# Kernel optimization log

Hardware: AMD Instinct MI355X
Metric: run time of the kernel (lower is better)

Reference implementation:

```python
import jax, jax.numpy as jnp
import numpy as np

V, E, U, D = 32000, 128, 256, 256
B, T = 128, 1024


def setup_inputs() -> dict:
    key = jax.random.key(0)
    k_tok, k_emb, k_wk, k_wr, k_wd = jax.random.split(key, 5)
    tokens = jax.random.randint(k_tok, (B, T), 0, V, dtype=jnp.int32)
    emb_table = jax.random.normal(k_emb, (V, E), dtype=jnp.float32) * 0.02
    Wk = jax.random.normal(k_wk, (E, 4 * U), dtype=jnp.float32) * (1.0 / np.sqrt(E))
    Wr = jax.random.normal(k_wr, (U, 4 * U), dtype=jnp.float32) * (1.0 / np.sqrt(U))
    # Keras unit_forget_bias: forget-gate bias initialized to ones (gate order i,f,g,o)
    b = jnp.concatenate([jnp.zeros((U,), jnp.float32), jnp.ones((U,), jnp.float32), jnp.zeros((2 * U,), jnp.float32)])
    Wd = jax.random.normal(k_wd, (U, D), dtype=jnp.float32) * (1.0 / np.sqrt(U))
    bd = jnp.zeros((D,), jnp.float32)
    return {"tokens": tokens, "emb_table": emb_table, "Wk": Wk, "Wr": Wr, "b": b, "Wd": Wd, "bd": bd}


def _masked_lstm(x, mask, Wk, Wr, b):
    # x: [B,T,E], mask: [B,T] bool. Keras semantics: masked steps pass
    # previous h as output and leave (h, c) unchanged.
    units = Wr.shape[0]
    bsz = x.shape[0]
    xT = jnp.swapaxes(x, 0, 1)          # [T,B,E]
    mT = jnp.swapaxes(mask, 0, 1)       # [T,B]

    def step(carry, inp):
        h, c = carry
        xt, mt = inp
        z = xt @ Wk + h @ Wr + b        # [B,4U]
        i, f, g, o = jnp.split(z, 4, axis=-1)
        i = jax.nn.sigmoid(i)
        f = jax.nn.sigmoid(f)
        g = jnp.tanh(g)
        o = jax.nn.sigmoid(o)
        c_new = f * c + i * g
        h_new = o * jnp.tanh(c_new)
        m = mt[:, None]
        h2 = jnp.where(m, h_new, h)
        c2 = jnp.where(m, c_new, c)
        return (h2, c2), h2

    h0 = jnp.zeros((bsz, units), x.dtype)
    c0 = jnp.zeros((bsz, units), x.dtype)
    _, outs = jax.lax.scan(step, (h0, c0), (xT, mT))
    return jnp.swapaxes(outs, 0, 1)     # [B,T,U]


def reference(tokens, emb_table, Wk, Wr, b, Wd, bd):
    # Embedding (mask_zero=True); dropout layers are identity at inference.
    x = emb_table[tokens]               # [B,T,E]
    mask = tokens != 0                  # [B,T]
    h = _masked_lstm(x, mask, Wk, Wr, b)  # [B,T,U]
    y = jax.nn.relu(h @ Wd + bd)        # TimeDistributed Dense(relu) -> [B,T,D]
    return y
```

## Files before the change

kernel.cpp:

```cpp
#include <hip/hip_runtime.h>
#include <cstddef>


typedef unsigned int u32x4 __attribute__((ext_vector_type(4)));

constexpr int TLEN = 1024;
constexpr int EDIM = 128;
constexpr int UDIM = 256;
constexpr int DDIM = 256;

constexpr int NBG  = 16;
constexpr int BPB  = 8;
constexpr int UPB  = 8;
constexpr int ZCOL = 32;
constexpr int HXROW = 432;
constexpr int ZROW = 36;

__device__ unsigned long long g_pktA[2][128][256];
__device__ unsigned long long g_pktB[2][128][256];
__device__ unsigned           g_cnt[NBG][32];

__device__ __forceinline__ int pidx(int k) { return ((k >> 5) * 36) + (k & 31); }

__device__ __forceinline__ u32x4 pkt_load_ic(const unsigned long long* p) {
  u32x4 v;
  asm volatile("global_load_dwordx4 %0, %1, off sc0 sc1" : "=v"(v) : "v"(p));
  return v;
}
__device__ __forceinline__ u32x4 pkt_load_l2(const unsigned long long* p) {
  u32x4 v;
  asm volatile("global_load_dwordx4 %0, %1, off sc0" : "=v"(v) : "v"(p));
  return v;
}
__device__ __forceinline__ unsigned cnt_load_ic(const unsigned* p) {
  unsigned v;
  asm volatile("global_load_dword %0, %1, off sc0 sc1" : "=v"(v) : "v"(p));
  asm volatile("s_waitcnt vmcnt(0)" : "+v"(v) :: "memory");
  return v;
}
#define PKT_WAIT4(a, b, c, d) \
  asm volatile("s_waitcnt vmcnt(0)" : "+v"(a), "+v"(b), "+v"(c), "+v"(d) :: "memory")
#define TAGS_OK() \
  ((p0[1] == want) & (p0[3] == want) & (p1[1] == want) & (p1[3] == want) & \
   (p2[1] == want) & (p2[3] == want) & (p3[1] == want) & (p3[3] == want))

__device__ __forceinline__ float rowsum16(float v) {
  v += __int_as_float(
      __builtin_amdgcn_mov_dpp(__float_as_int(v), 0x121, 0xf, 0xf, true));
  v += __int_as_float(
      __builtin_amdgcn_mov_dpp(__float_as_int(v), 0x122, 0xf, 0xf, true));
  v += __int_as_float(
      __builtin_amdgcn_mov_dpp(__float_as_int(v), 0x124, 0xf, 0xf, true));
  v += __int_as_float(
      __builtin_amdgcn_mov_dpp(__float_as_int(v), 0x128, 0xf, 0xf, true));
  return v;
}

__global__ void we_init() {
  const int i = blockIdx.x * 256 + threadIdx.x;
  if (i < NBG * 32)
    __hip_atomic_store(&(&g_cnt[0][0])[i], 0u, __ATOMIC_RELAXED,
                       __HIP_MEMORY_SCOPE_AGENT);
}

__global__ __launch_bounds__(256, 2) void we_lstm(
    const int* __restrict__ tokens, const float* __restrict__ emb,
    const float* __restrict__ Wk, const float* __restrict__ Wr,
    const float* __restrict__ bz, float* __restrict__ out)
{
  __shared__ float hx[2][BPB][HXROW];
  __shared__ float zs[BPB][ZROW];
  __shared__ float bias_s[ZCOL];

  const int tid = threadIdx.x;
  const int bid = blockIdx.x;
  const int bg  = ((bid & 7) << 1) | ((bid >> 8) & 1);
  const int ug  = (bid >> 3) & 31;
  const int b0  = bg * BPB;
  const int u0  = ug * UPB;

  const int ksl = tid & 15;
  const int cq  = (tid >> 4) & 7;
  const int bh  = tid >> 7;

  float w[96];
#pragma unroll
  for (int i = 0; i < 6; ++i)
#pragma unroll
    for (int j = 0; j < 4; ++j) {
      const int k = ksl * 4 + i * 64 + j;
#pragma unroll
      for (int cc = 0; cc < 4; ++cc) {
        const int c   = cq * 4 + cc;
        const int col = ((c >> 3) << 8) + u0 + (c & 7);
        w[(i * 4 + j) * 4 + cc] =
            (k < UDIM) ? Wr[k * 1024 + col] : Wk[(k - UDIM) * 1024 + col];
      }
    }
  if (tid < ZCOL) bias_s[tid] = bz[((tid >> 3) << 8) + u0 + (tid & 7)];

  float creg = 0.f;
  const int gb = tid >> 3, gu = tid & 7;
  const int xb = tid >> 5, xe = (tid & 31) << 2;
  const int up = tid & 127, bq = (tid >> 7) * 4;

  bool use_local = true;

  float4 xv = *(const float4*)&emb[(size_t)tokens[(b0 + xb) * TLEN] * EDIM + xe];
  int tk_g = (tid < 64) ? tokens[(b0 + gb) * TLEN] : 1;

  for (int it = 0; it < TLEN; ++it) {
    const int cur = it & 1;

    *(float4*)&hx[cur][xb][pidx(UDIM + xe)] = xv;
    __syncthreads();

    float acc[4][4];
#pragma unroll
    for (int r = 0; r < 4; ++r) {
      acc[r][0] = 0.f; acc[r][1] = 0.f; acc[r][2] = 0.f; acc[r][3] = 0.f;
    }
#pragma unroll
    for (int i = 4; i < 6; ++i) {
      const int hoff = pidx(ksl * 4 + i * 64);
      float4 hv[4];
#pragma unroll
      for (int r = 0; r < 4; ++r)
        hv[r] = *(const float4*)&hx[cur][bh * 4 + r][hoff];
#pragma unroll
      for (int j = 0; j < 4; ++j)
#pragma unroll
        for (int r = 0; r < 4; ++r) {
          const float hval = (j == 0) ? hv[r].x : (j == 1) ? hv[r].y
                             : (j == 2) ? hv[r].z : hv[r].w;
#pragma unroll
          for (int cc = 0; cc < 4; ++cc)
            acc[r][cc] += hval * w[(i * 4 + j) * 4 + cc];
        }
    }

    u32x4 p0, p1, p2, p3;
    const unsigned want = (unsigned)it;
    const int rp = (it + 1) & 1;
    if (it > 0) {
      if (use_local) {
        p0 = pkt_load_l2(&g_pktA[rp][b0 + bq + 0][2 * up]);
        p1 = pkt_load_l2(&g_pktA[rp][b0 + bq + 1][2 * up]);
        p2 = pkt_load_l2(&g_pktA[rp][b0 + bq + 2][2 * up]);
        p3 = pkt_load_l2(&g_pktA[rp][b0 + bq + 3][2 * up]);
      } else {
        p0 = pkt_load_ic(&g_pktB[rp][b0 + bq + 0][2 * up]);
        p1 = pkt_load_ic(&g_pktB[rp][b0 + bq + 1][2 * up]);
        p2 = pkt_load_ic(&g_pktB[rp][b0 + bq + 2][2 * up]);
        p3 = pkt_load_ic(&g_pktB[rp][b0 + bq + 3][2 * up]);
      }
    }

    float4 xv_n;
    int tk_g_n = 1;
    if (it + 1 < TLEN) {
      const int tk_x = tokens[(b0 + xb) * TLEN + it + 1];
      xv_n = *(const float4*)&emb[(size_t)tk_x * EDIM + xe];
      if (tid < 64) tk_g_n = tokens[(b0 + gb) * TLEN + it + 1];
    }

    const int ho = pidx(2 * up);
    if (it > 0) {
      PKT_WAIT4(p0, p1, p2, p3);
      bool ok = TAGS_OK();
      if (!ok) {
        const unsigned wantc = 32u * (unsigned)it;
        while (cnt_load_ic(&g_cnt[bg][0]) < wantc)
          __builtin_amdgcn_s_sleep(1);
        if (use_local) {
          p0 = pkt_load_l2(&g_pktA[rp][b0 + bq + 0][2 * up]);
          p1 = pkt_load_l2(&g_pktA[rp][b0 + bq + 1][2 * up]);
          p2 = pkt_load_l2(&g_pktA[rp][b0 + bq + 2][2 * up]);
          p3 = pkt_load_l2(&g_pktA[rp][b0 + bq + 3][2 * up]);
          PKT_WAIT4(p0, p1, p2, p3);
          ok = TAGS_OK();
          if (!ok) use_local = false;
        }
        while (!ok) {
          p0 = pkt_load_ic(&g_pktB[rp][b0 + bq + 0][2 * up]);
          p1 = pkt_load_ic(&g_pktB[rp][b0 + bq + 1][2 * up]);
          p2 = pkt_load_ic(&g_pktB[rp][b0 + bq + 2][2 * up]);
          p3 = pkt_load_ic(&g_pktB[rp][b0 + bq + 3][2 * up]);
          PKT_WAIT4(p0, p1, p2, p3);
          ok = TAGS_OK();
          if (!ok) __builtin_amdgcn_s_sleep(1);
        }
      }
      *(float2*)&hx[cur][bq + 0][ho] =
          make_float2(__uint_as_float(p0[0]), __uint_as_float(p0[2]));
      *(float2*)&hx[cur][bq + 1][ho] =
          make_float2(__uint_as_float(p1[0]), __uint_as_float(p1[2]));
      *(float2*)&hx[cur][bq + 2][ho] =
          make_float2(__uint_as_float(p2[0]), __uint_as_float(p2[2]));
      *(float2*)&hx[cur][bq + 3][ho] =
          make_float2(__uint_as_float(p3[0]), __uint_as_float(p3[2]));
    } else {
#pragma unroll
      for (int jj = 0; jj < 4; ++jj)
        *(float2*)&hx[cur][bq + jj][ho] = make_float2(0.f, 0.f);
    }
    __syncthreads();

#pragma unroll
    for (int i = 0; i < 4; ++i) {
      const int hoff = pidx(ksl * 4 + i * 64);
      float4 hv[4];
#pragma unroll
      for (int r = 0; r < 4; ++r)
        hv[r] = *(const float4*)&hx[cur][bh * 4 + r][hoff];
#pragma unroll
      for (int j = 0; j < 4; ++j)
#pragma unroll
        for (int r = 0; r < 4; ++r) {
          const float hval = (j == 0) ? hv[r].x : (j == 1) ? hv[r].y
                             : (j == 2) ? hv[r].z : hv[r].w;
#pragma unroll
          for (int cc = 0; cc < 4; ++cc)
            acc[r][cc] += hval * w[(i * 4 + j) * 4 + cc];
        }
    }

#pragma unroll
    for (int r = 0; r < 4; ++r)
#pragma unroll
      for (int cc = 0; cc < 4; ++cc)
        acc[r][cc] = rowsum16(acc[r][cc]);
    if (ksl == 0) {
#pragma unroll
      for (int r = 0; r < 4; ++r)
        *(float4*)&zs[bh * 4 + r][cq * 4] =
            make_float4(acc[r][0], acc[r][1], acc[r][2], acc[r][3]);
    }
    __syncthreads();

    if (tid < 64) {
      const float zi = zs[gb][gu]      + bias_s[gu];
      const float zf = zs[gb][8 + gu]  + bias_s[8 + gu];
      const float zg = zs[gb][16 + gu] + bias_s[16 + gu];
      const float zo = zs[gb][24 + gu] + bias_s[24 + gu];
      const float gi = 1.f / (1.f + __expf(-zi));
      const float gf = 1.f / (1.f + __expf(-zf));
      const float gg = 1.f - 2.f / (1.f + __expf(2.f * zg));
      const float go = 1.f / (1.f + __expf(-zo));
      const float cn = gf * creg + gi * gg;
      const float th = 1.f - 2.f / (1.f + __expf(2.f * cn));
      const float hn = go * th;
      const bool msk = (tk_g != 0);
      const float hold = hx[cur][gb][pidx(u0 + gu)];
      const float h2 = msk ? hn : hold;
      creg = msk ? cn : creg;
      const unsigned long long pkt =
          ((unsigned long long)(unsigned)(it + 1) << 32) | __float_as_uint(h2);
      __hip_atomic_store(&g_pktA[cur][b0 + gb][u0 + gu], pkt, __ATOMIC_RELAXED,
                         __HIP_MEMORY_SCOPE_WORKGROUP);
      __hip_atomic_store(&g_pktB[cur][b0 + gb][u0 + gu], pkt, __ATOMIC_RELAXED,
                         __HIP_MEMORY_SCOPE_AGENT);
      __builtin_nontemporal_store(
          h2, &out[((size_t)(b0 + gb) * TLEN + it) * DDIM + u0 + gu]);
      asm volatile("s_waitcnt vmcnt(0)" ::: "memory");
      if (tid == 0)
        __hip_atomic_fetch_add(&g_cnt[bg][0], 1u, __ATOMIC_RELAXED,
                               __HIP_MEMORY_SCOPE_AGENT);
    }
    xv = xv_n;
    tk_g = tk_g_n;
  }
}

__global__ __launch_bounds__(256, 2) void we_proj(
    const float* __restrict__ Wd, const float* __restrict__ bd,
    float* __restrict__ out)
{
  __shared__ float hs[32][260];
  __shared__ float ws[32][260];
  __shared__ float bds[DDIM];

  const int tid = threadIdx.x;
  const size_t row0 = (size_t)blockIdx.x * 32;

#pragma unroll
  for (int j2 = 0; j2 < 8; ++j2) {
    const int idx = tid + j2 * 256;
    const int r = idx >> 6;
    const int cq = idx & 63;
    *(float4*)&hs[r][cq * 4] = *(const float4*)&out[(row0 + r) * DDIM + cq * 4];
  }
  bds[tid] = bd[tid];

  const int rg = tid >> 5;
  const int c0 = (tid & 31) * 8;
  float acc[4][8];
#pragma unroll
  for (int i = 0; i < 4; ++i)
#pragma unroll
    for (int c = 0; c < 8; ++c) acc[i][c] = 0.f;

  for (int kt = 0; kt < 8; ++kt) {
    __syncthreads();
#pragma unroll
    for (int j2 = 0; j2 < 8; ++j2) {
      const int idx = tid + j2 * 256;
      const int kk = idx >> 6;
      const int cq = idx & 63;
      *(float4*)&ws[kk][cq * 4] =
          *(const float4*)&Wd[(size_t)(kt * 32 + kk) * DDIM + cq * 4];
    }
    __syncthreads();
#pragma unroll
    for (int kk = 0; kk < 32; ++kk) {
      const float4 wv0 = *(const float4*)&ws[kk][c0];
      const float4 wv1 = *(const float4*)&ws[kk][c0 + 4];
#pragma unroll
      for (int i = 0; i < 4; ++i) {
        const float hval = hs[rg + i * 8][kt * 32 + kk];
        acc[i][0] += hval * wv0.x; acc[i][1] += hval * wv0.y;
        acc[i][2] += hval * wv0.z; acc[i][3] += hval * wv0.w;
        acc[i][4] += hval * wv1.x; acc[i][5] += hval * wv1.y;
        acc[i][6] += hval * wv1.z; acc[i][7] += hval * wv1.w;
      }
    }
  }
#pragma unroll
  for (int i = 0; i < 4; ++i) {
    float4 y0, y1;
    y0.x = fmaxf(acc[i][0] + bds[c0 + 0], 0.f);
    y0.y = fmaxf(acc[i][1] + bds[c0 + 1], 0.f);
    y0.z = fmaxf(acc[i][2] + bds[c0 + 2], 0.f);
    y0.w = fmaxf(acc[i][3] + bds[c0 + 3], 0.f);
    y1.x = fmaxf(acc[i][4] + bds[c0 + 4], 0.f);
    y1.y = fmaxf(acc[i][5] + bds[c0 + 5], 0.f);
    y1.z = fmaxf(acc[i][6] + bds[c0 + 6], 0.f);
    y1.w = fmaxf(acc[i][7] + bds[c0 + 7], 0.f);
    const size_t orow = (row0 + rg + i * 8) * DDIM;
    *(float4*)&out[orow + c0]     = y0;
    *(float4*)&out[orow + c0 + 4] = y1;
  }
}

extern "C" void kernel_launch(void* const* d_in, const int* in_sizes, int n_in,
                              void* d_out, int out_size, void* d_ws, size_t ws_size,
                              hipStream_t stream) {
  const int*   tokens = (const int*)d_in[0];
  const float* emb    = (const float*)d_in[1];
  const float* Wk     = (const float*)d_in[2];
  const float* Wr     = (const float*)d_in[3];
  const float* bz     = (const float*)d_in[4];
  const float* Wd     = (const float*)d_in[5];
  const float* bd     = (const float*)d_in[6];
  float* out = (float*)d_out;
  (void)in_sizes; (void)n_in; (void)out_size; (void)d_ws; (void)ws_size;
  hipLaunchKernelGGL(we_init, dim3(2), dim3(256), 0, stream);
  hipLaunchKernelGGL(we_lstm, dim3(512), dim3(256), 0, stream,
                     tokens, emb, Wk, Wr, bz, out);
  hipLaunchKernelGGL(we_proj, dim3(128 * TLEN / 32), dim3(256), 0, stream,
                     Wd, bd, out);
}
```

Before: 3.650 ms.

## Compute gates in registers after reduction and split L2/IC ready counters

Reassigns weight columns so that after the DPP row reduction each lane with ksl<4 holds all four gates for one (batch, unit) pair. This removes the zs shared staging buffer and one __syncthreads per step. Readiness signalling is split into a workgroup-scope L2 counter and an agent-scope IC counter, each bumped per wavefront, with a bounded spin on the local counter before falling back to the coherent path. Half the blocks also sleep briefly at start to stagger them. The price is more atomics per step, each wavefront waiting on vmcnt twice, and more intricate fallback logic.

```diff
diff --git a/kernel.cpp b/kernel.cpp
--- a/kernel.cpp
+++ b/kernel.cpp
@@ -12,13 +12,12 @@
 constexpr int NBG  = 16;
 constexpr int BPB  = 8;
 constexpr int UPB  = 8;
-constexpr int ZCOL = 32;
 constexpr int HXROW = 432;
-constexpr int ZROW = 36;
 
 __device__ unsigned long long g_pktA[2][128][256];
 __device__ unsigned long long g_pktB[2][128][256];
-__device__ unsigned           g_cnt[NBG][32];
+__device__ unsigned           g_cntL[NBG][32];
+__device__ unsigned           g_cntIC[NBG][32];
 
 __device__ __forceinline__ int pidx(int k) { return ((k >> 5) * 36) + (k & 31); }
 
@@ -30,6 +29,12 @@
 __device__ __forceinline__ u32x4 pkt_load_l2(const unsigned long long* p) {
   u32x4 v;
   asm volatile("global_load_dwordx4 %0, %1, off sc0" : "=v"(v) : "v"(p));
+  return v;
+}
+__device__ __forceinline__ unsigned cnt_load_l2(const unsigned* p) {
+  unsigned v;
+  asm volatile("global_load_dword %0, %1, off sc0" : "=v"(v) : "v"(p));
+  asm volatile("s_waitcnt vmcnt(0)" : "+v"(v) :: "memory");
   return v;
 }
 __device__ __forceinline__ unsigned cnt_load_ic(const unsigned* p) {
@@ -58,9 +63,12 @@
 
 __global__ void we_init() {
   const int i = blockIdx.x * 256 + threadIdx.x;
-  if (i < NBG * 32)
-    __hip_atomic_store(&(&g_cnt[0][0])[i], 0u, __ATOMIC_RELAXED,
+  if (i < NBG * 32) {
+    __hip_atomic_store(&(&g_cntL[0][0])[i], 0u, __ATOMIC_RELAXED,
                        __HIP_MEMORY_SCOPE_AGENT);
+    __hip_atomic_store(&(&g_cntIC[0][0])[i], 0u, __ATOMIC_RELAXED,
+                       __HIP_MEMORY_SCOPE_AGENT);
+  }
 }
 
 __global__ __launch_bounds__(256, 2) void we_lstm(
@@ -69,8 +77,6 @@
     const float* __restrict__ bz, float* __restrict__ out)
 {
   __shared__ float hx[2][BPB][HXROW];
-  __shared__ float zs[BPB][ZROW];
-  __shared__ float bias_s[ZCOL];
 
   const int tid = threadIdx.x;
   const int bid = blockIdx.x;
@@ -91,23 +97,29 @@
       const int k = ksl * 4 + i * 64 + j;
 #pragma unroll
       for (int cc = 0; cc < 4; ++cc) {
-        const int c   = cq * 4 + cc;
-        const int col = ((c >> 3) << 8) + u0 + (c & 7);
+        const int col = (cc << 8) + u0 + cq;
         w[(i * 4 + j) * 4 + cc] =
             (k < UDIM) ? Wr[k * 1024 + col] : Wk[(k - UDIM) * 1024 + col];
       }
     }
-  if (tid < ZCOL) bias_s[tid] = bz[((tid >> 3) << 8) + u0 + (tid & 7)];
+  float bias_r[4];
+#pragma unroll
+  for (int cc = 0; cc < 4; ++cc) bias_r[cc] = bz[(cc << 8) + u0 + cq];
 
   float creg = 0.f;
-  const int gb = tid >> 3, gu = tid & 7;
+  const int gbat = bh * 4 + (tid & 3);
   const int xb = tid >> 5, xe = (tid & 31) << 2;
   const int up = tid & 127, bq = (tid >> 7) * 4;
 
   bool use_local = true;
 
   float4 xv = *(const float4*)&emb[(size_t)tokens[(b0 + xb) * TLEN] * EDIM + xe];
-  int tk_g = (tid < 64) ? tokens[(b0 + gb) * TLEN] : 1;
+  int tk_m = tokens[(b0 + gbat) * TLEN];
+
+  if ((bid >> 8) & 1) {
+    __builtin_amdgcn_s_sleep(31);
+    __builtin_amdgcn_s_sleep(31);
+  }
 
   for (int it = 0; it < TLEN; ++it) {
     const int cur = it & 1;
@@ -157,11 +169,11 @@
     }
 
     float4 xv_n;
-    int tk_g_n = 1;
+    int tk_m_n = 1;
     if (it + 1 < TLEN) {
       const int tk_x = tokens[(b0 + xb) * TLEN + it + 1];
       xv_n = *(const float4*)&emb[(size_t)tk_x * EDIM + xe];
-      if (tid < 64) tk_g_n = tokens[(b0 + gb) * TLEN + it + 1];
+      tk_m_n = tokens[(b0 + gbat) * TLEN + it + 1];
     }
 
     const int ho = pidx(2 * up);
@@ -169,26 +181,37 @@
       PKT_WAIT4(p0, p1, p2, p3);
       bool ok = TAGS_OK();
       if (!ok) {
-        const unsigned wantc = 32u * (unsigned)it;
-        while (cnt_load_ic(&g_cnt[bg][0]) < wantc)
-          __builtin_amdgcn_s_sleep(1);
+        const unsigned wantc = 128u * (unsigned)it;
         if (use_local) {
-          p0 = pkt_load_l2(&g_pktA[rp][b0 + bq + 0][2 * up]);
-          p1 = pkt_load_l2(&g_pktA[rp][b0 + bq + 1][2 * up]);
-          p2 = pkt_load_l2(&g_pktA[rp][b0 + bq + 2][2 * up]);
-          p3 = pkt_load_l2(&g_pktA[rp][b0 + bq + 3][2 * up]);
-          PKT_WAIT4(p0, p1, p2, p3);
-          ok = TAGS_OK();
+          int rounds = 0;
+          bool cert = false;
+          while (rounds < 64) {
+            if (cnt_load_l2(&g_cntL[bg][0]) >= wantc) { cert = true; break; }
+            __builtin_amdgcn_s_sleep(1);
+            ++rounds;
+          }
+          if (cert) {
+            p0 = pkt_load_l2(&g_pktA[rp][b0 + bq + 0][2 * up]);
+            p1 = pkt_load_l2(&g_pktA[rp][b0 + bq + 1][2 * up]);
+            p2 = pkt_load_l2(&g_pktA[rp][b0 + bq + 2][2 * up]);
+            p3 = pkt_load_l2(&g_pktA[rp][b0 + bq + 3][2 * up]);
+            PKT_WAIT4(p0, p1, p2, p3);
+            ok = TAGS_OK();
+          }
           if (!ok) use_local = false;
         }
-        while (!ok) {
-          p0 = pkt_load_ic(&g_pktB[rp][b0 + bq + 0][2 * up]);
-          p1 = pkt_load_ic(&g_pktB[rp][b0 + bq + 1][2 * up]);
-          p2 = pkt_load_ic(&g_pktB[rp][b0 + bq + 2][2 * up]);
-          p3 = pkt_load_ic(&g_pktB[rp][b0 + bq + 3][2 * up]);
-          PKT_WAIT4(p0, p1, p2, p3);
-          ok = TAGS_OK();
-          if (!ok) __builtin_amdgcn_s_sleep(1);
+        if (!ok) {
+          while (cnt_load_ic(&g_cntIC[bg][0]) < wantc)
+            __builtin_amdgcn_s_sleep(1);
+          do {
+            p0 = pkt_load_ic(&g_pktB[rp][b0 + bq + 0][2 * up]);
+            p1 = pkt_load_ic(&g_pktB[rp][b0 + bq + 1][2 * up]);
+            p2 = pkt_load_ic(&g_pktB[rp][b0 + bq + 2][2 * up]);
+            p3 = pkt_load_ic(&g_pktB[rp][b0 + bq + 3][2 * up]);
+            PKT_WAIT4(p0, p1, p2, p3);
+            ok = TAGS_OK();
+            if (!ok) __builtin_amdgcn_s_sleep(1);
+          } while (!ok);
         }
       }
       *(float2*)&hx[cur][bq + 0][ho] =
@@ -230,45 +253,47 @@
 #pragma unroll
       for (int cc = 0; cc < 4; ++cc)
         acc[r][cc] = rowsum16(acc[r][cc]);
-    if (ksl == 0) {
-#pragma unroll
-      for (int r = 0; r < 4; ++r)
-        *(float4*)&zs[bh * 4 + r][cq * 4] =
-            make_float4(acc[r][0], acc[r][1], acc[r][2], acc[r][3]);
-    }
-    __syncthreads();
-
-    if (tid < 64) {
-      const float zi = zs[gb][gu]      + bias_s[gu];
-      const float zf = zs[gb][8 + gu]  + bias_s[8 + gu];
-      const float zg = zs[gb][16 + gu] + bias_s[16 + gu];
-      const float zo = zs[gb][24 + gu] + bias_s[24 + gu];
-      const float gi = 1.f / (1.f + __expf(-zi));
-      const float gf = 1.f / (1.f + __expf(-zf));
-      const float gg = 1.f - 2.f / (1.f + __expf(2.f * zg));
-      const float go = 1.f / (1.f + __expf(-zo));
+
+    const bool pub = (ksl < 4);
+    unsigned long long pkt = 0;
+    float h2 = 0.f;
+    if (pub) {
+      float z4[4];
+#pragma unroll
+      for (int cc = 0; cc < 4; ++cc)
+        z4[cc] = ((ksl == 0) ? acc[0][cc] : (ksl == 1) ? acc[1][cc]
+                  : (ksl == 2) ? acc[2][cc] : acc[3][cc]) + bias_r[cc];
+      const float gi = 1.f / (1.f + __expf(-z4[0]));
+      const float gf = 1.f / (1.f + __expf(-z4[1]));
+      const float gg = 1.f - 2.f / (1.f + __expf(2.f * z4[2]));
+      const float go = 1.f / (1.f + __expf(-z4[3]));
       const float cn = gf * creg + gi * gg;
       const float th = 1.f - 2.f / (1.f + __expf(2.f * cn));
       const float hn = go * th;
-      const bool msk = (tk_g != 0);
-      const float hold = hx[cur][gb][pidx(u0 + gu)];
-      const float h2 = msk ? hn : hold;
+      const bool msk = (tk_m != 0);
+      const float hold = hx[cur][gbat][pidx(u0 + cq)];
+      h2 = msk ? hn : hold;
       creg = msk ? cn : creg;
-      const unsigned long long pkt =
-          ((unsigned long long)(unsigned)(it + 1) << 32) | __float_as_uint(h2);
-      __hip_atomic_store(&g_pktA[cur][b0 + gb][u0 + gu], pkt, __ATOMIC_RELAXED,
-                         __HIP_MEMORY_SCOPE_WORKGROUP);
-      __hip_atomic_store(&g_pktB[cur][b0 + gb][u0 + gu], pkt, __ATOMIC_RELAXED,
-                         __HIP_MEMORY_SCOPE_AGENT);
+      pkt = ((unsigned long long)(unsigned)(it + 1) << 32) | __float_as_uint(h2);
+      __hip_atomic_store(&g_pktA[cur][b0 + gbat][u0 + cq], pkt,
+                         __ATOMIC_RELAXED, __HIP_MEMORY_SCOPE_WORKGROUP);
+    }
+    asm volatile("s_waitcnt vmcnt(0)" ::: "memory");
+    if ((tid & 63) == 0)
+      __hip_atomic_fetch_add(&g_cntL[bg][0], 1u, __ATOMIC_RELAXED,
+                             __HIP_MEMORY_SCOPE_WORKGROUP);
+    if (pub)
+      __hip_atomic_store(&g_pktB[cur][b0 + gbat][u0 + cq], pkt,
+                         __ATOMIC_RELAXED, __HIP_MEMORY_SCOPE_AGENT);
+    asm volatile("s_waitcnt vmcnt(0)" ::: "memory");
+    if ((tid & 63) == 0)
+      __hip_atomic_fetch_add(&g_cntIC[bg][0], 1u, __ATOMIC_RELAXED,
+                             __HIP_MEMORY_SCOPE_AGENT);
+    if (pub)
       __builtin_nontemporal_store(
-          h2, &out[((size_t)(b0 + gb) * TLEN + it) * DDIM + u0 + gu]);
-      asm volatile("s_waitcnt vmcnt(0)" ::: "memory");
-      if (tid == 0)
-        __hip_atomic_fetch_add(&g_cnt[bg][0], 1u, __ATOMIC_RELAXED,
-                               __HIP_MEMORY_SCOPE_AGENT);
-    }
+          h2, &out[((size_t)(b0 + gbat) * TLEN + it) * DDIM + u0 + cq]);
     xv = xv_n;
-    tk_g = tk_g_n;
+    tk_m = tk_m_n;
   }
 }
 
```

After: 7.585 ms. 108% more time.

## Split step counter into local-L2 and cross-die counters for faster handoff

Applied to the files above, without the earlier changes.

Replaces the single agent-scope arrival counter with two counters. One is bumped right after the workgroup-scope (local L2) packet store and polled with L2-only loads for a bounded number of rounds. The other is the existing agent-scope counter, bumped after the coherent store and used as a fallback. The aim is to let consumers on the same XCD see readiness without waiting on the slower infinity-cache-coherent path. The cost is an extra waitcnt and atomic on the producer side per step, plus a bounded spin that may add latency when the producers are remote.

```diff
diff --git a/kernel.cpp b/kernel.cpp
--- a/kernel.cpp
+++ b/kernel.cpp
@@ -18,7 +18,8 @@
 
 __device__ unsigned long long g_pktA[2][128][256];
 __device__ unsigned long long g_pktB[2][128][256];
-__device__ unsigned           g_cnt[NBG][32];
+__device__ unsigned           g_cntL[NBG][32];
+__device__ unsigned           g_cntIC[NBG][32];
 
 __device__ __forceinline__ int pidx(int k) { return ((k >> 5) * 36) + (k & 31); }
 
@@ -30,6 +31,12 @@
 __device__ __forceinline__ u32x4 pkt_load_l2(const unsigned long long* p) {
   u32x4 v;
   asm volatile("global_load_dwordx4 %0, %1, off sc0" : "=v"(v) : "v"(p));
+  return v;
+}
+__device__ __forceinline__ unsigned cnt_load_l2(const unsigned* p) {
+  unsigned v;
+  asm volatile("global_load_dword %0, %1, off sc0" : "=v"(v) : "v"(p));
+  asm volatile("s_waitcnt vmcnt(0)" : "+v"(v) :: "memory");
   return v;
 }
 __device__ __forceinline__ unsigned cnt_load_ic(const unsigned* p) {
@@ -58,9 +65,12 @@
 
 __global__ void we_init() {
   const int i = blockIdx.x * 256 + threadIdx.x;
-  if (i < NBG * 32)
-    __hip_atomic_store(&(&g_cnt[0][0])[i], 0u, __ATOMIC_RELAXED,
+  if (i < NBG * 32) {
+    __hip_atomic_store(&(&g_cntL[0][0])[i], 0u, __ATOMIC_RELAXED,
                        __HIP_MEMORY_SCOPE_AGENT);
+    __hip_atomic_store(&(&g_cntIC[0][0])[i], 0u, __ATOMIC_RELAXED,
+                       __HIP_MEMORY_SCOPE_AGENT);
+  }
 }
 
 __global__ __launch_bounds__(256, 2) void we_lstm(
@@ -170,25 +180,36 @@
       bool ok = TAGS_OK();
       if (!ok) {
         const unsigned wantc = 32u * (unsigned)it;
-        while (cnt_load_ic(&g_cnt[bg][0]) < wantc)
-          __builtin_amdgcn_s_sleep(1);
         if (use_local) {
-          p0 = pkt_load_l2(&g_pktA[rp][b0 + bq + 0][2 * up]);
-          p1 = pkt_load_l2(&g_pktA[rp][b0 + bq + 1][2 * up]);
-          p2 = pkt_load_l2(&g_pktA[rp][b0 + bq + 2][2 * up]);
-          p3 = pkt_load_l2(&g_pktA[rp][b0 + bq + 3][2 * up]);
-          PKT_WAIT4(p0, p1, p2, p3);
-          ok = TAGS_OK();
+          int rounds = 0;
+          bool cert = false;
+          while (rounds < 96) {
+            if (cnt_load_l2(&g_cntL[bg][0]) >= wantc) { cert = true; break; }
+            __builtin_amdgcn_s_sleep(1);
+            ++rounds;
+          }
+          if (cert) {
+            p0 = pkt_load_l2(&g_pktA[rp][b0 + bq + 0][2 * up]);
+            p1 = pkt_load_l2(&g_pktA[rp][b0 + bq + 1][2 * up]);
+            p2 = pkt_load_l2(&g_pktA[rp][b0 + bq + 2][2 * up]);
+            p3 = pkt_load_l2(&g_pktA[rp][b0 + bq + 3][2 * up]);
+            PKT_WAIT4(p0, p1, p2, p3);
+            ok = TAGS_OK();
+          }
           if (!ok) use_local = false;
         }
-        while (!ok) {
-          p0 = pkt_load_ic(&g_pktB[rp][b0 + bq + 0][2 * up]);
-          p1 = pkt_load_ic(&g_pktB[rp][b0 + bq + 1][2 * up]);
-          p2 = pkt_load_ic(&g_pktB[rp][b0 + bq + 2][2 * up]);
-          p3 = pkt_load_ic(&g_pktB[rp][b0 + bq + 3][2 * up]);
-          PKT_WAIT4(p0, p1, p2, p3);
-          ok = TAGS_OK();
-          if (!ok) __builtin_amdgcn_s_sleep(1);
+        if (!ok) {
+          while (cnt_load_ic(&g_cntIC[bg][0]) < wantc)
+            __builtin_amdgcn_s_sleep(1);
+          do {
+            p0 = pkt_load_ic(&g_pktB[rp][b0 + bq + 0][2 * up]);
+            p1 = pkt_load_ic(&g_pktB[rp][b0 + bq + 1][2 * up]);
+            p2 = pkt_load_ic(&g_pktB[rp][b0 + bq + 2][2 * up]);
+            p3 = pkt_load_ic(&g_pktB[rp][b0 + bq + 3][2 * up]);
+            PKT_WAIT4(p0, p1, p2, p3);
+            ok = TAGS_OK();
+            if (!ok) __builtin_amdgcn_s_sleep(1);
+          } while (!ok);
         }
       }
       *(float2*)&hx[cur][bq + 0][ho] =
@@ -258,13 +279,17 @@
           ((unsigned long long)(unsigned)(it + 1) << 32) | __float_as_uint(h2);
       __hip_atomic_store(&g_pktA[cur][b0 + gb][u0 + gu], pkt, __ATOMIC_RELAXED,
                          __HIP_MEMORY_SCOPE_WORKGROUP);
+      asm volatile("s_waitcnt vmcnt(0)" ::: "memory");
+      if (tid == 0)
+        __hip_atomic_fetch_add(&g_cntL[bg][0], 1u, __ATOMIC_RELAXED,
+                               __HIP_MEMORY_SCOPE_WORKGROUP);
       __hip_atomic_store(&g_pktB[cur][b0 + gb][u0 + gu], pkt, __ATOMIC_RELAXED,
                          __HIP_MEMORY_SCOPE_AGENT);
       __builtin_nontemporal_store(
           h2, &out[((size_t)(b0 + gb) * TLEN + it) * DDIM + u0 + gu]);
       asm volatile("s_waitcnt vmcnt(0)" ::: "memory");
       if (tid == 0)
-        __hip_atomic_fetch_add(&g_cnt[bg][0], 1u, __ATOMIC_RELAXED,
+        __hip_atomic_fetch_add(&g_cntIC[bg][0], 1u, __ATOMIC_RELAXED,
                                __HIP_MEMORY_SCOPE_AGENT);
     }
     xv = xv_n;
```

New measurement: 4.084 ms. 1.12x slower.
